# Performance work log

Hardware: AMD Instinct MI355X
Metric: run time of the kernel (lower is better)

## Reference

```python
import jax, jax.numpy as jnp
import numpy as np

KL_W = 0.001
Q_W = 0.1

def setup_inputs() -> dict:
    key = jax.random.key(0)
    k1, k2, k3, k4 = jax.random.split(key, 4)
    B, N, M, L = 2, 4096, 4096, 512
    return {
        'pred': jax.random.normal(k1, (B, N, 3), dtype=jnp.float32),
        'target': jax.random.normal(k2, (B, M, 3), dtype=jnp.float32),
        'mu': jax.random.normal(k3, (B, L), dtype=jnp.float32),
        'logvar': jax.random.normal(k4, (B, L), dtype=jnp.float32),
    }

def reference(pred, target, mu, logvar):
    # Chamfer distance: pairwise squared distances [B, N, M] then min-reductions
    d_pt = jnp.sum((pred[:, :, None, :] - target[:, None, :, :]) ** 2, axis=-1)
    cd = (d_pt.min(axis=2).mean(axis=1) + d_pt.min(axis=1).mean(axis=1)).mean()

    # KL divergence of diagonal Gaussian vs standard normal
    kl = -0.5 * jnp.mean(1.0 + logvar - mu ** 2 - jnp.exp(logvar))

    # Density uniformity: nearest-neighbor self-distance std (unbiased, like torch.std)
    d_pp = jnp.sum((pred[:, :, None, :] - pred[:, None, :, :]) ** 2, axis=-1)
    N = pred.shape[1]
    d_pp = d_pp + jnp.eye(N, dtype=pred.dtype)[None] * 1e6  # mask self-distance
    nn_dist = d_pp.min(axis=2)  # [B, N]
    density = jnp.std(nn_dist, axis=1, ddof=1).mean()

    total = cd + KL_W * kl + Q_W * density
    return total, cd, kl, density
```

## Files before the change

kernel.cpp:

```cpp
#include <hip/hip_runtime.h>
#include <hip/hip_bf16.h>
#include <math.h>

constexpr int B = 2;
constexpr int N = 4096;
constexpr int M = 4096;
constexpr int L = 512;

constexpr float KL_W = 0.001f;
constexpr float Q_W  = 0.1f;

constexpr int THREADS = 256;
constexpr int QPT     = 2;
constexpr int QC      = THREADS * QPT;
constexpr int DT      = 256;
constexpr int GX      = N / QC;
constexpr int GY      = M / DT;
constexpr int GZ      = 3 * B;

constexpr size_t MINS_BYTES = (size_t)3 * B * N * 4;

__global__ __launch_bounds__(THREADS) void mgl_pairmin_kernel(
    const float* __restrict__ pred, const float* __restrict__ target,
    unsigned* __restrict__ mins)
{
    __shared__ float4 tile[DT];

    const int z   = blockIdx.z;
    const int dir = z >> 1;
    const int b   = z & 1;

    const float* qb; const float* db; unsigned* ob;
    if (dir == 0)      { qb = pred   + b * N * 3; db = target + b * M * 3; ob = mins + (0 * B + b) * N; }
    else if (dir == 1) { qb = target + b * M * 3; db = pred   + b * N * 3; ob = mins + (1 * B + b) * N; }
    else               { qb = pred   + b * N * 3; db = pred   + b * N * 3; ob = mins + (2 * B + b) * N; }

    const int q0 = blockIdx.x * QC;
    const int d0 = blockIdx.y * DT;

    {
        const float* p = db + (size_t)(d0 + threadIdx.x) * 3;
        float x = p[0], y = p[1], zz = p[2];
        tile[threadIdx.x] = make_float4(x, y, zz, fmaf(x, x, fmaf(y, y, zz * zz)));
    }

    const int qi0 = q0 + threadIdx.x;
    const int qi1 = qi0 + THREADS;

    const float qx0 = qb[qi0 * 3 + 0], qy0 = qb[qi0 * 3 + 1], qz0 = qb[qi0 * 3 + 2];
    const float qx1 = qb[qi1 * 3 + 0], qy1 = qb[qi1 * 3 + 1], qz1 = qb[qi1 * 3 + 2];
    const float qw0 = fmaf(qx0, qx0, fmaf(qy0, qy0, qz0 * qz0));
    const float qw1 = fmaf(qx1, qx1, fmaf(qy1, qy1, qz1 * qz1));
    const float ax0 = -2.0f * qx0, ay0 = -2.0f * qy0, az0 = -2.0f * qz0;
    const float ax1 = -2.0f * qx1, ay1 = -2.0f * qy1, az1 = -2.0f * qz1;

    __syncthreads();

    float m0 = 3.402823466e+38f;
    float m1 = 3.402823466e+38f;

    if (dir != 2) {
        #pragma unroll 8
        for (int j = 0; j < DT; ++j) {
            float4 t = tile[j];
            float v0 = fmaf(ax0, t.x, fmaf(ay0, t.y, fmaf(az0, t.z, t.w)));
            float v1 = fmaf(ax1, t.x, fmaf(ay1, t.y, fmaf(az1, t.z, t.w)));
            m0 = fminf(m0, v0);
            m1 = fminf(m1, v1);
        }
    } else {
        #pragma unroll 8
        for (int j = 0; j < DT; ++j) {
            float4 t = tile[j];
            const int dj = d0 + j;
            float v0 = fmaf(ax0, t.x, fmaf(ay0, t.y, fmaf(az0, t.z, t.w)));
            float v1 = fmaf(ax1, t.x, fmaf(ay1, t.y, fmaf(az1, t.z, t.w)));
            v0 = (dj == qi0) ? 3.402823466e+38f : v0;
            v1 = (dj == qi1) ? 3.402823466e+38f : v1;
            m0 = fminf(m0, v0);
            m1 = fminf(m1, v1);
        }
    }

    m0 = fmaxf(m0 + qw0, 0.0f);
    m1 = fmaxf(m1 + qw1, 0.0f);

    atomicMin(ob + qi0, __float_as_uint(m0));
    atomicMin(ob + qi1, __float_as_uint(m1));
}

__global__ __launch_bounds__(256) void mgl_finalize_kernel(
    const unsigned* __restrict__ mins, const float* __restrict__ mu,
    const float* __restrict__ logvar, float* __restrict__ out)
{
    const int tid = threadIdx.x;

    double sPT[B], sTP[B], sPP[B], ssPP[B];
    #pragma unroll
    for (int bb = 0; bb < B; ++bb) { sPT[bb] = 0.0; sTP[bb] = 0.0; sPP[bb] = 0.0; ssPP[bb] = 0.0; }
    double skl = 0.0;

    #pragma unroll
    for (int bb = 0; bb < B; ++bb) {
        for (int i = tid; i < N; i += 256) {
            double vpt = (double)__uint_as_float(mins[(0 * B + bb) * N + i]);
            double vtp = (double)__uint_as_float(mins[(1 * B + bb) * N + i]);
            double vpp = (double)__uint_as_float(mins[(2 * B + bb) * N + i]);
            sPT[bb]  += vpt;
            sTP[bb]  += vtp;
            sPP[bb]  += vpp;
            ssPP[bb] += vpp * vpp;
        }
    }
    for (int i = tid; i < B * L; i += 256) {
        double m  = (double)mu[i];
        double lv = (double)logvar[i];
        skl += 1.0 + lv - m * m - exp(lv);
    }

    __shared__ double red[9][256];
    red[0][tid] = sPT[0]; red[1][tid] = sPT[1];
    red[2][tid] = sTP[0]; red[3][tid] = sTP[1];
    red[4][tid] = sPP[0]; red[5][tid] = sPP[1];
    red[6][tid] = ssPP[0]; red[7][tid] = ssPP[1];
    red[8][tid] = skl;
    __syncthreads();
    for (int s = 128; s > 0; s >>= 1) {
        if (tid < s) {
            #pragma unroll
            for (int k = 0; k < 9; ++k) red[k][tid] += red[k][tid + s];
        }
        __syncthreads();
    }

    if (tid == 0) {
        double cd = 0.0;
        #pragma unroll
        for (int bb = 0; bb < B; ++bb)
            cd += red[0 + bb][0] / (double)N + red[2 + bb][0] / (double)M;
        cd /= (double)B;

        double density = 0.0;
        #pragma unroll
        for (int bb = 0; bb < B; ++bb) {
            double s  = red[4 + bb][0];
            double ss = red[6 + bb][0];
            double var = (ss - s * s / (double)N) / (double)(N - 1);
            density += sqrt(var > 0.0 ? var : 0.0);
        }
        density /= (double)B;

        double kl = -0.5 * red[8][0] / (double)(B * L);

        double total = cd + (double)KL_W * kl + (double)Q_W * density;
        out[0] = (float)total;
        out[1] = (float)cd;
        out[2] = (float)kl;
        out[3] = (float)density;
    }
}

extern "C" void kernel_launch(void* const* d_in, const int* in_sizes, int n_in,
                              void* d_out, int out_size, void* d_ws, size_t ws_size,
                              hipStream_t stream) {
    const float* pred   = (const float*)d_in[0];
    const float* target = (const float*)d_in[1];
    const float* mu     = (const float*)d_in[2];
    const float* logvar = (const float*)d_in[3];
    float* out = (float*)d_out;

    unsigned* mins = (unsigned*)d_ws;

    hipMemsetAsync(mins, 0x7F, MINS_BYTES, stream);
    mgl_pairmin_kernel<<<dim3(GX, GY, GZ), THREADS, 0, stream>>>(pred, target, mins);
    mgl_finalize_kernel<<<1, 256, 0, stream>>>(mins, mu, logvar, out);
}
```

Measured before the change: 81.65 us.

## Replace atomicMin and memset with per-tile partial minima reduced in finalize

The pair-min kernel now writes each block's per-query minimum into its own slice of a partial buffer (one slice per data tile) instead of issuing global atomicMin into a memset-initialised array. This drops the memset launch and the atomic contention. The finalize kernel grows to 1024 threads, reduces the 16 partial slices with float4 loads, and replaces the shared-memory tree with wave shuffles. The cost is a larger workspace (16x the minima), a heavier single-block finalize pass, and reliance on ws_size being large enough.

```diff
diff --git a/kernel.cpp b/kernel.cpp
--- a/kernel.cpp
+++ b/kernel.cpp
@@ -18,11 +18,10 @@
 constexpr int GY      = M / DT;
 constexpr int GZ      = 3 * B;
 
-constexpr size_t MINS_BYTES = (size_t)3 * B * N * 4;
 
 __global__ __launch_bounds__(THREADS) void mgl_pairmin_kernel(
     const float* __restrict__ pred, const float* __restrict__ target,
-    unsigned* __restrict__ mins)
+    float* __restrict__ partial)
 {
     __shared__ float4 tile[DT];
 
@@ -30,10 +29,10 @@
     const int dir = z >> 1;
     const int b   = z & 1;
 
-    const float* qb; const float* db; unsigned* ob;
-    if (dir == 0)      { qb = pred   + b * N * 3; db = target + b * M * 3; ob = mins + (0 * B + b) * N; }
-    else if (dir == 1) { qb = target + b * M * 3; db = pred   + b * N * 3; ob = mins + (1 * B + b) * N; }
-    else               { qb = pred   + b * N * 3; db = pred   + b * N * 3; ob = mins + (2 * B + b) * N; }
+    const float* qb; const float* db;
+    if (dir == 0)      { qb = pred   + b * N * 3; db = target + b * M * 3; }
+    else if (dir == 1) { qb = target + b * M * 3; db = pred   + b * N * 3; }
+    else               { qb = pred   + b * N * 3; db = pred   + b * N * 3; }
 
     const int q0 = blockIdx.x * QC;
     const int d0 = blockIdx.y * DT;
@@ -85,12 +84,15 @@
     m0 = fmaxf(m0 + qw0, 0.0f);
     m1 = fmaxf(m1 + qw1, 0.0f);
 
-    atomicMin(ob + qi0, __float_as_uint(m0));
-    atomicMin(ob + qi1, __float_as_uint(m1));
+    float* slice = partial + ((size_t)blockIdx.y * GZ + z) * N;
+    slice[qi0] = m0;
+    slice[qi1] = m1;
 }
 
-__global__ __launch_bounds__(256) void mgl_finalize_kernel(
-    const unsigned* __restrict__ mins, const float* __restrict__ mu,
+constexpr int FT = 1024;
+
+__global__ __launch_bounds__(FT) void mgl_finalize_kernel(
+    const float* __restrict__ partial, const float* __restrict__ mu,
     const float* __restrict__ logvar, float* __restrict__ out)
 {
     const int tid = threadIdx.x;
@@ -100,57 +102,77 @@
     for (int bb = 0; bb < B; ++bb) { sPT[bb] = 0.0; sTP[bb] = 0.0; sPP[bb] = 0.0; ssPP[bb] = 0.0; }
     double skl = 0.0;
 
-    #pragma unroll
-    for (int bb = 0; bb < B; ++bb) {
-        for (int i = tid; i < N; i += 256) {
-            double vpt = (double)__uint_as_float(mins[(0 * B + bb) * N + i]);
-            double vtp = (double)__uint_as_float(mins[(1 * B + bb) * N + i]);
-            double vpp = (double)__uint_as_float(mins[(2 * B + bb) * N + i]);
-            sPT[bb]  += vpt;
-            sTP[bb]  += vtp;
-            sPP[bb]  += vpp;
-            ssPP[bb] += vpp * vpp;
+    for (int t = tid; t < GZ * (N / 4); t += FT) {
+        const int z  = t / (N / 4);
+        const int q4 = (t % (N / 4)) * 4;
+        const float4* p = (const float4*)(partial + (size_t)z * N + q4);
+        float4 m = p[0];
+        #pragma unroll
+        for (int gy = 1; gy < GY; ++gy) {
+            float4 v = p[(size_t)gy * GZ * N / 4];
+            m.x = fminf(m.x, v.x); m.y = fminf(m.y, v.y);
+            m.z = fminf(m.z, v.z); m.w = fminf(m.w, v.w);
+        }
+        const int dir = z >> 1;
+        const int bb  = z & 1;
+        double s = (double)m.x + (double)m.y + (double)m.z + (double)m.w;
+        if (dir == 0)      sPT[bb] += s;
+        else if (dir == 1) sTP[bb] += s;
+        else {
+            sPP[bb]  += s;
+            ssPP[bb] += (double)m.x * m.x + (double)m.y * m.y
+                      + (double)m.z * m.z + (double)m.w * m.w;
         }
     }
-    for (int i = tid; i < B * L; i += 256) {
-        double m  = (double)mu[i];
-        double lv = (double)logvar[i];
-        skl += 1.0 + lv - m * m - exp(lv);
+
+    if (tid < B * L) {
+        double m  = (double)mu[tid];
+        double lv = (double)logvar[tid];
+        skl = 1.0 + lv - m * m - exp(lv);
     }
 
-    __shared__ double red[9][256];
-    red[0][tid] = sPT[0]; red[1][tid] = sPT[1];
-    red[2][tid] = sTP[0]; red[3][tid] = sTP[1];
-    red[4][tid] = sPP[0]; red[5][tid] = sPP[1];
-    red[6][tid] = ssPP[0]; red[7][tid] = ssPP[1];
-    red[8][tid] = skl;
-    __syncthreads();
-    for (int s = 128; s > 0; s >>= 1) {
-        if (tid < s) {
-            #pragma unroll
-            for (int k = 0; k < 9; ++k) red[k][tid] += red[k][tid + s];
-        }
-        __syncthreads();
+    double acc[9] = { sPT[0], sPT[1], sTP[0], sTP[1], sPP[0], sPP[1], ssPP[0], ssPP[1], skl };
+    #pragma unroll
+    for (int k = 0; k < 9; ++k) {
+        #pragma unroll
+        for (int off = 32; off > 0; off >>= 1)
+            acc[k] += __shfl_down(acc[k], off, 64);
     }
 
+    __shared__ double wred[FT / 64][9];
+    const int wid  = tid >> 6;
+    const int lane = tid & 63;
+    if (lane == 0) {
+        #pragma unroll
+        for (int k = 0; k < 9; ++k) wred[wid][k] = acc[k];
+    }
+    __syncthreads();
+
     if (tid == 0) {
+        double tot[9];
+        #pragma unroll
+        for (int k = 0; k < 9; ++k) tot[k] = wred[0][k];
+        for (int w = 1; w < FT / 64; ++w)
+            #pragma unroll
+            for (int k = 0; k < 9; ++k) tot[k] += wred[w][k];
+
         double cd = 0.0;
         #pragma unroll
         for (int bb = 0; bb < B; ++bb)
-            cd += red[0 + bb][0] / (double)N + red[2 + bb][0] / (double)M;
+            cd += tot[0 + bb] / (double)N + tot[2 + bb] / (double)M;
         cd /= (double)B;
 
         double density = 0.0;
         #pragma unroll
         for (int bb = 0; bb < B; ++bb) {
-            double s  = red[4 + bb][0];
-            double ss = red[6 + bb][0];
+            double s  = tot[4 + bb];
+            double ss = tot[6 + bb];
             double var = (ss - s * s / (double)N) / (double)(N - 1);
             density += sqrt(var > 0.0 ? var : 0.0);
         }
         density /= (double)B;
 
-        double kl = -0.5 * red[8][0] / (double)(B * L);
+        double kl = -0.5 * tot[8] / (double)(B * L);
 
         double total = cd + (double)KL_W * kl + (double)Q_W * density;
         out[0] = (float)total;
@@ -169,9 +191,8 @@
     const float* logvar = (const float*)d_in[3];
     float* out = (float*)d_out;
 
-    unsigned* mins = (unsigned*)d_ws;
+    float* partial = (float*)d_ws;
 
-    hipMemsetAsync(mins, 0x7F, MINS_BYTES, stream);
-    mgl_pairmin_kernel<<<dim3(GX, GY, GZ), THREADS, 0, stream>>>(pred, target, mins);
-    mgl_finalize_kernel<<<1, 256, 0, stream>>>(mins, mu, logvar, out);
+    mgl_pairmin_kernel<<<dim3(GX, GY, GZ), THREADS, 0, stream>>>(pred, target, partial);
+    mgl_finalize_kernel<<<1, FT, 0, stream>>>(partial, mu, logvar, out);
 }
```

New measurement: 100.1 us. 1.23x slower.
